# Kernel optimization log

Measured on AMD Instinct MI355X. Metric: run time of the kernel, lower is better.

The kernel has to match this reference:

```python
import jax, jax.numpy as jnp
import numpy as np

B, C, Hh, Ww = 32, 512, 6, 40
NC = 97   # num classes; padding_idx = NC-1, start_idx = NC-2
L = 26    # label length (max_len+1); decoder tokens T = L+1 = 27


def _lstm2(x, layers):
    """2-layer unidirectional LSTM, batch_first, PyTorch gate order (i,f,g,o).
    x: (B,T,D); layers: list of (Wih, Whh, bih, bhh). Returns (B,T,H)."""
    h = x
    for (Wih, Whh, bih, bhh) in layers:
        Hd = Whh.shape[1]
        b = bih + bhh
        def step(carry, xt, Wih=Wih, Whh=Whh, b=b):
            hh, cc = carry
            g = xt @ Wih.T + hh @ Whh.T + b
            i, f, gg, o = jnp.split(g, 4, axis=-1)
            cc = jax.nn.sigmoid(f) * cc + jax.nn.sigmoid(i) * jnp.tanh(gg)
            hh = jax.nn.sigmoid(o) * jnp.tanh(cc)
            return (hh, cc), hh
        init = (jnp.zeros((h.shape[0], Hd), h.dtype), jnp.zeros((h.shape[0], Hd), h.dtype))
        _, ys = jax.lax.scan(step, init, jnp.swapaxes(h, 0, 1))
        h = jnp.swapaxes(ys, 0, 1)
    return h


def setup_inputs() -> dict:
    key = jax.random.key(0)
    it = iter(jax.random.split(key, 48))
    def nrm(shape, s=0.02):
        return jax.random.normal(next(it), shape, jnp.float32) * s
    d = {}
    d['feat'] = jax.random.normal(next(it), (B, C, Hh, Ww), jnp.float32)
    d['label'] = jax.random.randint(next(it), (B, L), 0, NC)
    d['valid_ratios'] = jax.random.uniform(next(it), (B,), jnp.float32, 0.5, 1.0)
    # encoder LSTM (2 layers, 512->512)
    for p in ['e0', 'e1']:
        d[p + '_Wih'] = nrm((4 * C, C)); d[p + '_Whh'] = nrm((4 * C, C))
        d[p + '_bih'] = jnp.zeros((4 * C,), jnp.float32); d[p + '_bhh'] = jnp.zeros((4 * C,), jnp.float32)
    d['enc_W'] = nrm((C, C)); d['enc_b'] = jnp.zeros((C,), jnp.float32)
    # attention: query 1x1 (Linear), key conv3x3, score 1x1 (Linear d->1)
    d['q_W'] = nrm((C, C)); d['q_b'] = jnp.zeros((C,), jnp.float32)
    d['k_W'] = nrm((C, C, 3, 3)); d['k_b'] = jnp.zeros((C,), jnp.float32)
    d['s_W'] = nrm((1, C)); d['s_b'] = jnp.zeros((1,), jnp.float32)
    emb = nrm((NC, C), 1.0)
    d['emb'] = emb.at[NC - 1].set(0.0)  # padding_idx row is zero
    # decoder LSTM (2 layers, 512->512)
    for p in ['d0', 'd1']:
        d[p + '_Wih'] = nrm((4 * C, C)); d[p + '_Whh'] = nrm((4 * C, C))
        d[p + '_bih'] = jnp.zeros((4 * C,), jnp.float32); d[p + '_bhh'] = jnp.zeros((4 * C,), jnp.float32)
    d['pred_W'] = nrm((NC, 3 * C)); d['pred_b'] = jnp.zeros((NC,), jnp.float32)
    return d


def reference(feat, label, valid_ratios,
              e0_Wih, e0_Whh, e0_bih, e0_bhh, e1_Wih, e1_Whh, e1_bih, e1_bhh,
              enc_W, enc_b, q_W, q_b, k_W, k_b, s_W, s_b, emb,
              d0_Wih, d0_Whh, d0_bih, d0_bhh, d1_Wih, d1_Whh, d1_bih, d1_bhh,
              pred_W, pred_b):
    # --- SAREncoder: max-pool over height, 2-layer LSTM, linear on last step ---
    feat_v = jnp.max(feat, axis=2).transpose(0, 2, 1)  # (B, W, C)
    hf = _lstm2(feat_v, [(e0_Wih, e0_Whh, e0_bih, e0_bhh), (e1_Wih, e1_Whh, e1_bih, e1_bhh)])
    holistic = hf[:, -1, :] @ enc_W.T + enc_b  # (B, C)
    # --- tokens: [holistic, embed(label)] ---
    tok = jnp.concatenate([holistic[:, None, :], emb[label]], axis=1)  # (B, T=L+1, C)
    Hid = _lstm2(tok, [(d0_Wih, d0_Whh, d0_bih, d0_bhh), (d1_Wih, d1_Whh, d1_bih, d1_bhh)])
    # --- 2D additive attention ---
    q = Hid @ q_W.T + q_b  # (B, T, C)
    k = jax.lax.conv_general_dilated(feat, k_W, (1, 1), 'SAME',
                                     dimension_numbers=('NCHW', 'OIHW', 'NCHW')) + k_b[None, :, None, None]
    t = jnp.tanh(k[:, None] + q[:, :, :, None, None])  # (B, T, C, h, w) big intermediate
    score = jnp.einsum('btchw,c->bthw', t, s_W[0]) + s_b[0]  # (B, T, h, w)
    vw = jnp.minimum(Ww, jnp.ceil(Ww * valid_ratios)).astype(jnp.int32)  # (B,)
    colmask = jnp.arange(Ww)[None, :] >= vw[:, None]  # (B, w)
    score = jnp.where(colmask[:, None, None, :], -jnp.inf, score)
    T = score.shape[1]
    aw = jax.nn.softmax(score.reshape(score.shape[0], T, -1), axis=-1).reshape(score.shape[0], T, Hh, Ww)
    attn_feat = jnp.einsum('bchw,bthw->btc', feat, aw)  # (B, T, C)
    # --- prediction (pred_concat=True); dropout is identity (deterministic) ---
    hol = jnp.broadcast_to(holistic[:, None, :], Hid.shape)
    preds = jnp.concatenate([Hid, attn_feat, hol], axis=-1) @ pred_W.T + pred_b
    return preds[:, 1:, :]  # (B, L, NC)
```

## Files before the change

kernel.cpp:

```cpp
#include <hip/hip_runtime.h>

typedef unsigned short u16;
typedef __attribute__((ext_vector_type(8))) short short8;
typedef __attribute__((ext_vector_type(4))) float floatx4;
typedef _Float16 half8 __attribute__((ext_vector_type(8)));
typedef _Float16 half2v __attribute__((ext_vector_type(2)));
typedef unsigned uint4v __attribute__((ext_vector_type(4)));

#define AGENT __HIP_MEMORY_SCOPE_AGENT
#define SENT 0x7FFF7FFFu

__device__ __forceinline__ float bf2f(u16 v) { return __uint_as_float(((unsigned)v) << 16); }
__device__ __forceinline__ u16 f2bf(float f) {
    unsigned u = __float_as_uint(f);
    unsigned r = (u + 0x7FFFu + ((u >> 16) & 1u)) >> 16;
    return (u16)r;
}
__device__ __forceinline__ float sigm_(float x) {
    return __builtin_amdgcn_rcpf(1.f + __expf(-x));
}
__device__ __forceinline__ float tanh_(float x) {
    x = fminf(fmaxf(x, -15.f), 15.f);
    float e = __expf(2.f * x);
    return (e - 1.f) * __builtin_amdgcn_rcpf(e + 1.f);
}

typedef __attribute__((address_space(1))) void gvoid_t;
typedef __attribute__((address_space(3))) void lvoid_t;
__device__ __forceinline__ void gl_lds16(const void* g, void* l) {
    __builtin_amdgcn_global_load_lds((gvoid_t*)g, (lvoid_t*)l, 16, 0, 0);
}

#define HEX_WORDS (134 * 32 * 256)

__global__ void init_k(const void* __restrict__ feat_raw, int* __restrict__ flag,
                       unsigned* __restrict__ hEx) {
    int idx = blockIdx.x * 256 + threadIdx.x;
    hEx[idx] = SENT;
    if (idx == 0) {
        const u16* p = (const u16*)feat_raw;
        int insane = 0;
        #pragma unroll
        for (int i = 0; i < 32; i += 2) {
            float x = bf2f(p[i]);
            float a = fabsf(x);
            if (!(a <= 1000.f)) insane = 1;
            if (x != 0.f && a < 1e-8f) insane = 1;
        }
        *flag = insane;
    }
}

struct SrcPtrs {
    const void* e0Wih; const void* e1Wih; const void* d0Wih; const void* d1Wih;
    const void* b0; const void* b1; const void* b2; const void* b3;
    const void* b4; const void* b5; const void* b6; const void* b7;
    const void* encW; const void* qW; const void* predW; const void* emb;
    const void* encb; const void* qb; const void* kb; const void* sW;
    const void* sb; const void* predb;
};
#define OFF_W0      0
#define OFF_W1      1048576
#define OFF_W2      2097152
#define OFF_W3      3145728
#define OFF_B       4194304
#define OFF_ENCW    4210688
#define OFF_QW      4472832
#define OFF_PREDW   4734976
#define OFF_EMB     4883968
#define OFF_ENCB    4933632
#define OFF_QB      4934144
#define OFF_KB      4934656
#define OFF_SW      4935168
#define OFF_SB      4935680
#define OFF_PREDB   4935681
#define CANON_TOTAL 4935778

__global__ __launch_bounds__(256) void canon_all(SrcPtrs S, u16* __restrict__ dst,
                                                 const int* __restrict__ flag) {
    int idx = blockIdx.x * 256 + threadIdx.x;
    if (idx >= CANON_TOTAL) return;
    const void* s; int loc;
    if (idx < OFF_B) {
        int k = idx >> 20; loc = idx & 1048575;
        s = (k == 0) ? S.e0Wih : (k == 1) ? S.e1Wih : (k == 2) ? S.d0Wih : S.d1Wih;
    } else if (idx < OFF_ENCW) {
        int r = idx - OFF_B; int k = r >> 11; loc = r & 2047;
        s = (k == 0) ? S.b0 : (k == 1) ? S.b1 : (k == 2) ? S.b2 : (k == 3) ? S.b3
          : (k == 4) ? S.b4 : (k == 5) ? S.b5 : (k == 6) ? S.b6 : S.b7;
    } else if (idx < OFF_QW)    { s = S.encW;  loc = idx - OFF_ENCW; }
    else if (idx < OFF_PREDW)   { s = S.qW;    loc = idx - OFF_QW; }
    else if (idx < OFF_EMB)     { s = S.predW; loc = idx - OFF_PREDW; }
    else if (idx < OFF_ENCB)    { s = S.emb;   loc = idx - OFF_EMB; }
    else if (idx < OFF_QB)      { s = S.encb;  loc = idx - OFF_ENCB; }
    else if (idx < OFF_KB)      { s = S.qb;    loc = idx - OFF_QB; }
    else if (idx < OFF_SW)      { s = S.kb;    loc = idx - OFF_KB; }
    else if (idx < OFF_SB)      { s = S.sW;    loc = idx - OFF_SW; }
    else if (idx < OFF_PREDB)   { s = S.sb;    loc = idx - OFF_SB; }
    else                        { s = S.predb; loc = idx - OFF_PREDB; }
    dst[idx] = (*flag) ? f2bf(((const float*)s)[loc]) : ((const u16*)s)[loc];
}

__global__ __launch_bounds__(64) void canonf_k(const void* __restrict__ src, float* __restrict__ dst,
                                               int n, const int* __restrict__ flag) {
    int i = blockIdx.x * 64 + threadIdx.x;
    if (i >= n) return;
    dst[i] = (*flag) ? ((const float*)src)[i] : bf2f(((const u16*)src)[i]);
}

__device__ __forceinline__ float rdf(const void* p, long i, int fl) {
    return fl ? ((const float*)p)[i] : bf2f(((const u16*)p)[i]);
}

__global__ __launch_bounds__(256) void featv_k(const void* __restrict__ feat, u16* __restrict__ featv,
                                               const int* __restrict__ flag) {
    const int fl = *flag;
    int idx = blockIdx.x * 256 + threadIdx.x;
    int c = idx & 511;
    int r = idx >> 9;
    int w = r % 40, b = r / 40;
    float mx = -1e30f;
    long base = ((long)(b * 512 + c) * 6) * 40 + w;
    #pragma unroll
    for (int h = 0; h < 6; h++) mx = fmaxf(mx, rdf(feat, base + h * 40, fl));
    featv[idx] = f2bf(mx);
}

__global__ __launch_bounds__(256) void padfeat_k(const void* __restrict__ feat, u16* __restrict__ featP,
                                                 const int* __restrict__ flag) {
    const int fl = *flag;
    int idx = blockIdx.x * 256 + threadIdx.x;
    int c = idx & 511;
    int r = idx >> 9;
    int wp = r % 42; int r2 = r / 42;
    int hp = r2 & 7; int b = r2 >> 3;
    u16 v = 0;
    if (hp >= 1 && hp <= 6 && wp >= 1 && wp <= 40) {
        long si = ((long)(b * 512 + c) * 6 + (hp - 1)) * 40 + (wp - 1);
        v = fl ? f2bf(((const float*)feat)[si]) : ((const u16*)feat)[si];
    }
    featP[idx] = v;
}

__global__ __launch_bounds__(256) void w2_k(const void* __restrict__ kW, u16* __restrict__ W2,
                                            const int* __restrict__ flag) {
    int idx = blockIdx.x * 256 + threadIdx.x;
    int co = idx / 4608;
    int r = idx % 4608;
    int kh = r / 1536;
    int r2 = r % 1536;
    int kw = r2 / 512;
    int ci = r2 & 511;
    long si = ((long)(co * 512 + ci) * 3 + kh) * 3 + kw;
    W2[idx] = (*flag) ? f2bf(((const float*)kW)[si]) : ((const u16*)kW)[si];
}

__global__ __launch_bounds__(256) void wq3_all(
    const void* __restrict__ s0, const void* __restrict__ s1,
    const void* __restrict__ s2, const void* __restrict__ s3,
    _Float16* __restrict__ d0, _Float16* __restrict__ d1,
    _Float16* __restrict__ d2, _Float16* __restrict__ d3,
    const int* __restrict__ flag)
{
    int gb = blockIdx.x;
    int id = gb >> 9;
    const void* W = (id == 0) ? s0 : (id == 1) ? s1 : (id == 2) ? s2 : s3;
    _Float16* D = (id == 0) ? d0 : (id == 1) ? d1 : (id == 2) ? d2 : d3;
    int o = (gb & 511) * 256 + threadIdx.x;
    int t = o & 511;
    int c = (o >> 9) & 31;
    int j = o >> 14;
    int rid = t >> 1, hf = t & 1;
    int n = (rid >> 6) * 512 + j * 64 + (rid & 63);
    int k = hf * 256 + c * 8;
    int fl = *flag;
    _Float16* dst = D + (long)o * 8;
    #pragma unroll
    for (int jj = 0; jj < 8; jj++) {
        long si = (long)n * 512 + k + jj;
        float v = fl ? ((const float*)W)[si] : bf2f(((const u16*)W)[si]);
        dst[jj] = (_Float16)v;
    }
}

__global__ __launch_bounds__(256) void gemm_nt_f32(
    const u16* __restrict__ A, int lda,
    const u16* __restrict__ Bw,
    const u16* __restrict__ bias0, const u16* __restrict__ bias1,
    float* __restrict__ C, int M, int N, int K, int ldc)
{
    __shared__ __align__(16) u16 As[64][40];
    __shared__ __align__(16) u16 Bs[64][40];
    const int tid = threadIdx.x;
    const int bn = blockIdx.x, bm = blockIdx.y;
    const int l = tid & 63, wid = tid >> 6;
    const int wm = wid >> 1, wn = wid & 1;
    const int lr = tid >> 2, lc = (tid & 3) * 8;
    const int l15 = l & 15, lq = l >> 4;

    floatx4 acc00 = (floatx4)(0.f), acc01 = (floatx4)(0.f), acc10 = (floatx4)(0.f), acc11 = (floatx4)(0.f);

    int am = bm * 64 + lr; if (am > M - 1) am = M - 1;
    const u16* Ap = A + (long)am * lda + lc;
    const u16* Bp = Bw + (long)(bn * 64 + lr) * K + lc;

    for (int k0 = 0; k0 < K; k0 += 32) {
        *(short8*)&As[lr][lc] = *(const short8*)(Ap + k0);
        *(short8*)&Bs[lr][lc] = *(const short8*)(Bp + k0);
        __syncthreads();
        short8 af0 = *(const short8*)&As[wm * 32 + l15][lq * 8];
        short8 af1 = *(const short8*)&As[wm * 32 + 16 + l15][lq * 8];
        short8 bf0 = *(const short8*)&Bs[wn * 32 + l15][lq * 8];
        short8 bf1 = *(const short8*)&Bs[wn * 32 + 16 + l15][lq * 8];
        acc00 = __builtin_amdgcn_mfma_f32_16x16x32_bf16(af0, bf0, acc00, 0, 0, 0);
        acc01 = __builtin_amdgcn_mfma_f32_16x16x32_bf16(af0, bf1, acc01, 0, 0, 0);
        acc10 = __builtin_amdgcn_mfma_f32_16x16x32_bf16(af1, bf0, acc10, 0, 0, 0);
        acc11 = __builtin_amdgcn_mfma_f32_16x16x32_bf16(af1, bf1, acc11, 0, 0, 0);
        __syncthreads();
    }
    floatx4 accs[2][2] = {{acc00, acc01}, {acc10, acc11}};
    #pragma unroll
    for (int i = 0; i < 2; i++)
        #pragma unroll
        for (int j = 0; j < 2; j++)
            #pragma unroll
            for (int r = 0; r < 4; r++) {
                int gm = bm * 64 + wm * 32 + i * 16 + lq * 4 + r;
                int gn = bn * 64 + wn * 32 + j * 16 + l15;
                if (gm < M) {
                    float v = accs[i][j][r];
                    if (bias0) v += bf2f(bias0[gn]);
                    if (bias1) v += bf2f(bias1[gn]);
                    C[(long)gm * ldc + gn] = v;
                }
            }
}

__global__ __launch_bounds__(256) void conv_gemm(
    const u16* __restrict__ featP, const u16* __restrict__ W2,
    const u16* __restrict__ kb, u16* __restrict__ kmap)
{
    __shared__ __align__(16) u16 As[2][128][32];
    __shared__ __align__(16) u16 Bs[2][128][32];
    const int tid = threadIdx.x;
    int bm = blockIdx.x * 8 + (blockIdx.y & 7);
    int bn = blockIdx.y >> 3;
    if (bm >= 60) return;
    const int wv = tid >> 6, l = tid & 63;
    const int wm = wv >> 1, wn = wv & 1;
    const int l15 = l & 15, lq = l >> 4;
    const int s0 = wv * 2, s1 = s0 + 1;

    int ar0 = bm * 128 + s0 * 16 + (l >> 2);
    int ar1 = bm * 128 + s1 * 16 + (l >> 2);
    int ab0 = ar0 / 240, ahw0 = ar0 % 240;
    int ab1 = ar1 / 240, ahw1 = ar1 % 240;
    const u16* ga0 = featP + ((long)(ab0 * 8 + ahw0 / 40) * 42 + (ahw0 % 40)) * 512 + (l & 3) * 8;
    const u16* ga1 = featP + ((long)(ab1 * 8 + ahw1 / 40) * 42 + (ahw1 % 40)) * 512 + (l & 3) * 8;
    const u16* gb0 = W2 + (long)(bn * 128 + s0 * 16 + (l >> 2)) * 4608 + (l & 3) * 8;
    const u16* gb1 = W2 + (long)(bn * 128 + s1 * 16 + (l >> 2)) * 4608 + (l & 3) * 8;

    floatx4 acc[4][4];
    #pragma unroll
    for (int i = 0; i < 4; i++)
        #pragma unroll
        for (int j = 0; j < 4; j++) acc[i][j] = (floatx4)(0.f);

    auto stage = [&](int k0, int pb) {
        int kh = k0 / 1536;
        int rem = k0 - kh * 1536;
        int aoff = (kh * 42 + (rem >> 9)) * 512 + (rem & 511);
        gl_lds16(ga0 + aoff, &As[pb][s0 * 16][0]);
        gl_lds16(ga1 + aoff, &As[pb][s1 * 16][0]);
        gl_lds16(gb0 + k0, &Bs[pb][s0 * 16][0]);
        gl_lds16(gb1 + k0, &Bs[pb][s1 * 16][0]);
    };

    stage(0, 0);
    __syncthreads();
    for (int k = 0; k < 144; k++) {
        int cur = k & 1;
        if (k + 1 < 144) stage((k + 1) * 32, cur ^ 1);
        short8 af[4], bf[4];
        #pragma unroll
        for (int i = 0; i < 4; i++) af[i] = *(const short8*)&As[cur][wm * 64 + i * 16 + l15][lq * 8];
        #pragma unroll
        for (int j = 0; j < 4; j++) bf[j] = *(const short8*)&Bs[cur][wn * 64 + j * 16 + l15][lq * 8];
        #pragma unroll
        for (int i = 0; i < 4; i++)
            #pragma unroll
            for (int j = 0; j < 4; j++)
                acc[i][j] = __builtin_amdgcn_mfma_f32_16x16x32_bf16(af[i], bf[j], acc[i][j], 0, 0, 0);
        __syncthreads();
    }

    #pragma unroll
    for (int i = 0; i < 4; i++)
        #pragma unroll
        for (int j = 0; j < 4; j++)
            #pragma unroll
            for (int r = 0; r < 4; r++) {
                int row = bm * 128 + wm * 64 + i * 16 + lq * 4 + r;
                int col = bn * 128 + wn * 64 + j * 16 + l15;
                kmap[(long)row * 512 + col] = f2bf(acc[i][j][r] + bf2f(kb[col]));
            }
}

#define WL(F) F(0) F(1) F(2) F(3) F(4) F(5) F(6) F(7) F(8) F(9) F(10) F(11) F(12) F(13) F(14) F(15) \
              F(16) F(17) F(18) F(19) F(20) F(21) F(22) F(23) F(24) F(25) F(26) F(27) F(28) F(29) F(30) F(31)
#define WLA(F) F(0,0) F(1,1) F(2,2) F(3,3) F(4,0) F(5,1) F(6,2) F(7,3) \
               F(8,0) F(9,1) F(10,2) F(11,3) F(12,0) F(13,1) F(14,2) F(15,3) \
               F(16,0) F(17,1) F(18,2) F(19,3) F(20,0) F(21,1) F(22,2) F(23,3) \
               F(24,0) F(25,1) F(26,2) F(27,3) F(28,0) F(29,1) F(30,2) F(31,3)
#define WDECL(i) half8 w##i = wp8[(long)(j * 32 + i) * 512 + tid];
#define WPIN(i)  asm volatile("" : "+v"(w##i));
#define DOTC(i,k) { \
    half8 hv = *(const half8*)&hS2[(hf * 2 + (i / 16)) * 136 + (i % 16) * 8]; \
    a##k = __builtin_amdgcn_fdot2(__builtin_shufflevector(hv, hv, 0, 1), __builtin_shufflevector(w##i, w##i, 0, 1), a##k, false); \
    a##k = __builtin_amdgcn_fdot2(__builtin_shufflevector(hv, hv, 2, 3), __builtin_shufflevector(w##i, w##i, 2, 3), a##k, false); \
    a##k = __builtin_amdgcn_fdot2(__builtin_shufflevector(hv, hv, 4, 5), __builtin_shufflevector(w##i, w##i, 4, 5), a##k, false); \
    a##k = __builtin_amdgcn_fdot2(__builtin_shufflevector(hv, hv, 6, 7), __builtin_shufflevector(w##i, w##i, 6, 7), a##k, false); }

__global__ __launch_bounds__(512) __attribute__((amdgpu_waves_per_eu(2, 2))) void lstm_sync(
    const float* __restrict__ xpre, const _Float16* __restrict__ Wq3,
    u16* __restrict__ seq_out, float* __restrict__ f32_out,
    unsigned* __restrict__ hExT, int T, int f32_ld)
{
    const int i_ = blockIdx.x;
    const int slot = i_ >> 3;
    const int b = (i_ & 7) * 4 + (slot & 3);
    const int j = slot >> 2;
    const int tid = threadIdx.x;
    const int hf = tid & 1;

    __shared__ __align__(16) _Float16 hS2[4 * 136];
    __shared__ float part[512];

    const half8* wp8 = (const half8*)Wq3;
    WL(WDECL)
    WL(WPIN)
    float cst = 0.f;

    for (int t = 0; t < T; t++) {
        float xi = 0.f, xf = 0.f, xg = 0.f, xo = 0.f;
        if (tid < 64) {
            const float* xp = xpre + ((long)b * T + t) * 2048 + j * 64 + tid;
            xi = xp[0]; xf = xp[512]; xg = xp[1024]; xo = xp[1536];
        }
        float a0 = 0.f, a1 = 0.f, a2 = 0.f, a3 = 0.f;
        if (t > 0) {
            if (tid < 64) {
                const unsigned* src = &hExT[((long)(t - 1) * 32 + b) * 256 + tid * 4];
                unsigned v0, v1, v2, v3;
                do {
                    v0 = __hip_atomic_load(src + 0, __ATOMIC_RELAXED, AGENT);
                    v1 = __hip_atomic_load(src + 1, __ATOMIC_RELAXED, AGENT);
                    v2 = __hip_atomic_load(src + 2, __ATOMIC_RELAXED, AGENT);
                    v3 = __hip_atomic_load(src + 3, __ATOMIC_RELAXED, AGENT);
                } while (v0 == SENT || v1 == SENT || v2 == SENT || v3 == SENT);
                uint4v v; v.x = v0; v.y = v1; v.z = v2; v.w = v3;
                *(uint4v*)&hS2[(tid >> 4) * 136 + (tid & 15) * 8] = v;
            }
            __syncthreads();
            WLA(DOTC)
        }
        part[tid] = (a0 + a1) + (a2 + a3);
        __syncthreads();
        if (tid < 64) {
            float gi = xi + part[(0   + tid) * 2] + part[(0   + tid) * 2 + 1];
            float gf = xf + part[(64  + tid) * 2] + part[(64  + tid) * 2 + 1];
            float gg = xg + part[(128 + tid) * 2] + part[(128 + tid) * 2 + 1];
            float go = xo + part[(192 + tid) * 2] + part[(192 + tid) * 2 + 1];
            cst = sigm_(gf) * cst + sigm_(gi) * tanh_(gg);
            float h = sigm_(go) * tanh_(cst);
            float hlo = __shfl(h, tid * 2);
            float hhi = __shfl(h, tid * 2 + 1);
            if (t + 1 < T && tid < 32) {
                half2v hp; hp[0] = (_Float16)hlo; hp[1] = (_Float16)hhi;
                __hip_atomic_store(&hExT[((long)t * 32 + b) * 256 + j * 32 + tid],
                                   *(unsigned*)&hp, __ATOMIC_RELAXED, AGENT);
            }
            asm volatile("" ::: "memory");
            long so = ((long)b * T + t) * 512 + j * 64 + tid;
            seq_out[so] = f2bf(h);
            if (f32_out) f32_out[((long)b * T + t) * f32_ld + j * 64 + tid] = h;
        }
    }
}

__global__ __launch_bounds__(256) void tok_k(
    const float* __restrict__ holf, const u16* __restrict__ cemb,
    const int* __restrict__ label, u16* __restrict__ tok)
{
    int idx = blockIdx.x * 256 + threadIdx.x;
    int c = idx & 511;
    int m = idx >> 9;
    int b = m / 27, t = m % 27;
    float v;
    if (t == 0) v = holf[(long)b * 512 + c];
    else v = bf2f(cemb[(long)label[b * 26 + (t - 1)] * 512 + c]);
    tok[idx] = f2bf(v);
}

__global__ __launch_bounds__(256) void score_k(
    const float* __restrict__ q, const u16* __restrict__ kmap,
    const u16* __restrict__ sW, const u16* __restrict__ sb,
    const float* __restrict__ vr, float* __restrict__ aw)
{
    int blk = blockIdx.x;
    int xcd = blk & 7, rest = blk >> 3;
    int bq = rest & 3, t = rest >> 2;
    int b = xcd * 4 + bq;
    int bt = b * 27 + t;
    int tid = threadIdx.x, wv = tid >> 6, ln = tid & 63;

    __shared__ float sc[240];
    __shared__ float red[256];

    float qr[8], sr[8];
    const float* qp = q + (long)bt * 512 + ln * 8;
    #pragma unroll
    for (int i = 0; i < 8; i++) qr[i] = qp[i];
    #pragma unroll
    for (int i = 0; i < 8; i++) sr[i] = bf2f(sW[ln * 8 + i]);

    const u16* kb_ = kmap + (long)b * 240 * 512;
    for (int r = wv * 60; r < wv * 60 + 60; r++) {
        short8 kv = *(const short8*)(kb_ + (long)r * 512 + ln * 8);
        float acc = 0.f;
        #pragma unroll
        for (int i = 0; i < 8; i++) {
            float x = bf2f((u16)kv[i]) + qr[i];
            acc = fmaf(sr[i], tanh_(x), acc);
        }
        #pragma unroll
        for (int m = 32; m > 0; m >>= 1) acc += __shfl_xor(acc, m);
        if (ln == 0) sc[r] = acc;
    }
    __syncthreads();

    float scv = -INFINITY, ex = 0.f;
    if (tid < 240) {
        float rr = vr[b];
        int vw = (int)ceilf(40.f * rr);
        if (vw > 40) vw = 40;
        int wcol = tid % 40;
        scv = (wcol >= vw) ? -INFINITY : (sc[tid] + bf2f(sb[0]));
    }
    red[tid] = scv;
    __syncthreads();
    for (int s = 128; s > 0; s >>= 1) {
        if (tid < s) red[tid] = fmaxf(red[tid], red[tid + s]);
        __syncthreads();
    }
    float mx = red[0];
    __syncthreads();
    if (tid < 240) ex = (scv == -INFINITY) ? 0.f : __expf(scv - mx);
    red[tid] = ex;
    __syncthreads();
    for (int s = 128; s > 0; s >>= 1) {
        if (tid < s) red[tid] += red[tid + s];
        __syncthreads();
    }
    float inv = __builtin_amdgcn_rcpf(red[0]);
    if (tid < 240) aw[(long)bt * 240 + tid] = ex * inv;
}

__global__ __launch_bounds__(256) void attn_k(
    const void* __restrict__ feat, const float* __restrict__ aw,
    float* __restrict__ concat, const int* __restrict__ flag)
{
    const int fl = *flag;
    int b = blockIdx.x >> 3;
    int cc = (blockIdx.x & 7) * 64;
    int tid = threadIdx.x;
    __shared__ float awS[27 * 240];
    __shared__ u16 fS[64 * 240];
    for (int i = tid; i < 27 * 240; i += 256) awS[i] = aw[(long)b * 27 * 240 + i];
    long fbase = ((long)b * 512 + cc) * 240;
    for (int i = tid; i < 64 * 240; i += 256)
        fS[i] = fl ? f2bf(((const float*)feat)[fbase + i]) : ((const u16*)feat)[fbase + i];
    __syncthreads();
    for (int item = tid; item < 64 * 27; item += 256) {
        int c = item / 27, t = item % 27;
        const u16* fp = &fS[c * 240];
        const float* ap = &awS[t * 240];
        float acc = 0.f;
        for (int hw = 0; hw < 240; hw++) acc = fmaf(bf2f(fp[hw]), ap[hw], acc);
        concat[((long)(b * 27 + t)) * 1536 + 512 + cc + c] = acc;
    }
}

__global__ __launch_bounds__(256) void pred_k(
    const float* __restrict__ concat, const float* __restrict__ holf,
    const u16* __restrict__ pW, const u16* __restrict__ pb,
    void* __restrict__ out, const int* __restrict__ flag)
{
    int m0 = blockIdx.x * 4;
    int tid = threadIdx.x;
    const int fl = *flag;
    __shared__ float aS[4][1024];
    __shared__ float hS[4][512];
    for (int i = tid; i < 4 * 1024; i += 256)
        aS[i / 1024][i % 1024] = concat[(long)(m0 + i / 1024) * 1536 + (i % 1024)];
    for (int i = tid; i < 4 * 512; i += 256) {
        int m = m0 + i / 512;
        hS[i / 512][i % 512] = holf[(long)(m / 27) * 512 + (i % 512)];
    }
    __syncthreads();
    int r = tid >> 6;
    int nb = tid & 63;
    int m = m0 + r;
    int b = m / 27, t = m % 27;
    for (int n = nb; n < 97; n += 64) {
        const u16* wp = pW + (long)n * 1536;
        float acc = 0.f;
        for (int k = 0; k < 1024; k++) acc = fmaf(aS[r][k], bf2f(wp[k]), acc);
        for (int k = 0; k < 512; k++) acc = fmaf(hS[r][k], bf2f(wp[1024 + k]), acc);
        acc += bf2f(pb[n]);
        if (t > 0) {
            long o = ((long)(b * 26 + (t - 1))) * 97 + n;
            if (fl) ((float*)out)[o] = acc;
            else    ((u16*)out)[o] = f2bf(acc);
        }
    }
}

extern "C" void kernel_launch(void* const* d_in, const int* in_sizes, int n_in,
                              void* d_out, int out_size, void* d_ws, size_t ws_size,
                              hipStream_t stream) {
    (void)in_sizes; (void)n_in; (void)out_size; (void)ws_size;
    const void* feat_r = d_in[0];
    const int*  label  = (const int*)d_in[1];
    const void* vr_r   = d_in[2];

    char* w = (char*)d_ws;
    size_t off = 0;
    auto alloc = [&](size_t bytes) -> void* {
        void* p = w + off;
        off = (off + bytes + 63) & ~(size_t)63;
        return p;
    };
    int*   flag    = (int*)  alloc(4);
    unsigned* hEx  = (unsigned*)alloc((size_t)HEX_WORDS * 4);
    u16*   canon   = (u16*)  alloc((size_t)CANON_TOTAL * 2);
    float* cvr     = (float*)alloc(32ull * 4);
    u16*   featv   = (u16*)  alloc(655360ull * 2);
    float* xpre    = (float*)alloc(2621440ull * 4);
    u16*   seq0    = (u16*)  alloc(655360ull * 2);
    u16*   seq1    = (u16*)  alloc(655360ull * 2);
    u16*   tok     = (u16*)  alloc(442368ull * 2);
    u16*   seqd0   = (u16*)  alloc(442368ull * 2);
    u16*   Hid     = (u16*)  alloc(442368ull * 2);
    float* holf    = (float*)alloc(16384ull * 4);
    float* qf      = (float*)alloc(442368ull * 4);
    u16*   featP   = (u16*)  alloc(5505024ull * 2);
    u16*   W2      = (u16*)  alloc(2359296ull * 2);
    float* aw      = (float*)alloc(207360ull * 4);
    float* concat  = (float*)alloc(1327104ull * 4);
    _Float16* Wq[4];
    for (int i = 0; i < 4; i++) Wq[i] = (_Float16*)alloc(1048576ull * 2);
    u16*   kmap    = (u16*)xpre;

    unsigned* hEx0 = hEx;
    unsigned* hEx1 = hEx + 40ull * 8192;
    unsigned* hEx2 = hEx + 80ull * 8192;
    unsigned* hEx3 = hEx + 107ull * 8192;

    u16* cW0    = canon + OFF_W0;
    u16* cW1    = canon + OFF_W1;
    u16* cW2    = canon + OFF_W2;
    u16* cW3    = canon + OFF_W3;
    u16* cb0    = canon + OFF_B;
    u16* cencW  = canon + OFF_ENCW;
    u16* cqW    = canon + OFF_QW;
    u16* cpredW = canon + OFF_PREDW;
    u16* cemb   = canon + OFF_EMB;
    u16* cencb  = canon + OFF_ENCB;
    u16* cqb    = canon + OFF_QB;
    u16* ckb    = canon + OFF_KB;
    u16* csW    = canon + OFF_SW;
    u16* csb    = canon + OFF_SB;
    u16* cpredb = canon + OFF_PREDB;

    init_k<<<dim3(HEX_WORDS / 256), 256, 0, stream>>>(feat_r, flag, hEx);
    SrcPtrs S;
    S.e0Wih = d_in[3];  S.e1Wih = d_in[7];  S.d0Wih = d_in[20]; S.d1Wih = d_in[24];
    S.b0 = d_in[5];  S.b1 = d_in[6];  S.b2 = d_in[9];  S.b3 = d_in[10];
    S.b4 = d_in[22]; S.b5 = d_in[23]; S.b6 = d_in[26]; S.b7 = d_in[27];
    S.encW = d_in[11]; S.qW = d_in[13]; S.predW = d_in[28]; S.emb = d_in[19];
    S.encb = d_in[12]; S.qb = d_in[14]; S.kb = d_in[16]; S.sW = d_in[17];
    S.sb = d_in[18]; S.predb = d_in[29];
    canon_all<<<dim3((CANON_TOTAL + 255) / 256), 256, 0, stream>>>(S, canon, flag);
    canonf_k<<<dim3(1), 64, 0, stream>>>(vr_r, cvr, 32, flag);
    w2_k<<<dim3(9216), 256, 0, stream>>>(d_in[15], W2, flag);
    wq3_all<<<dim3(2048), 256, 0, stream>>>(d_in[4], d_in[8], d_in[21], d_in[25],
                                            Wq[0], Wq[1], Wq[2], Wq[3], flag);

    featv_k  <<<dim3(2560), 256, 0, stream>>>(feat_r, featv, flag);
    padfeat_k<<<dim3(21504), 256, 0, stream>>>(feat_r, featP, flag);

    gemm_nt_f32<<<dim3(32, 20), 256, 0, stream>>>(featv, 512, cW0, cb0 + 0 * 2048, cb0 + 1 * 2048, xpre, 1280, 2048, 512, 2048);
    lstm_sync<<<dim3(256), 512, 0, stream>>>(xpre, Wq[0], seq0, nullptr, hEx0, 40, 0);
    gemm_nt_f32<<<dim3(32, 20), 256, 0, stream>>>(seq0, 512, cW1, cb0 + 2 * 2048, cb0 + 3 * 2048, xpre, 1280, 2048, 512, 2048);
    lstm_sync<<<dim3(256), 512, 0, stream>>>(xpre, Wq[1], seq1, nullptr, hEx1, 40, 0);
    gemm_nt_f32<<<dim3(8, 1), 256, 0, stream>>>(seq1 + 39 * 512, 40 * 512, cencW, cencb, nullptr, holf, 32, 512, 512, 512);

    tok_k<<<dim3(1728), 256, 0, stream>>>(holf, cemb, label, tok);
    gemm_nt_f32<<<dim3(32, 14), 256, 0, stream>>>(tok, 512, cW2, cb0 + 4 * 2048, cb0 + 5 * 2048, xpre, 864, 2048, 512, 2048);
    lstm_sync<<<dim3(256), 512, 0, stream>>>(xpre, Wq[2], seqd0, nullptr, hEx2, 27, 0);
    gemm_nt_f32<<<dim3(32, 14), 256, 0, stream>>>(seqd0, 512, cW3, cb0 + 6 * 2048, cb0 + 7 * 2048, xpre, 864, 2048, 512, 2048);
    lstm_sync<<<dim3(256), 512, 0, stream>>>(xpre, Wq[3], Hid, concat, hEx3, 27, 1536);

    gemm_nt_f32<<<dim3(8, 14), 256, 0, stream>>>(Hid, 512, cqW, cqb, nullptr, qf, 864, 512, 512, 512);
    conv_gemm<<<dim3(8, 32), 256, 0, stream>>>(featP, W2, ckb, kmap);
    score_k<<<dim3(864), 256, 0, stream>>>(qf, kmap, csW, csb, cvr, aw);
    attn_k<<<dim3(256), 256, 0, stream>>>(feat_r, aw, concat, flag);

    pred_k<<<dim3(216), 256, 0, stream>>>(concat, holf, cpredW, cpredb, d_out, flag);
}
```

Measured before the change: 841.5 us.

## Deepen conv GEMM LDS pipeline to four stages and swizzle LDS layout

The conv_gemm kernel moves from double-buffered LDS staging to a four-buffer ring with three loads in flight. It waits with explicit vmcnt counters and a single barrier per iteration instead of two syncthreads. An XOR swizzle on the 16-byte chunk index is applied to both the global-to-LDS writes and the MFMA operand reads, to reduce LDS bank conflicts. In exchange LDS use doubles to 64KB per block, which may lower occupancy, and the hand-tuned waitcnt values must match the number of loads each stage issues.

```diff
diff --git a/kernel.cpp b/kernel.cpp
--- a/kernel.cpp
+++ b/kernel.cpp
@@ -240,8 +240,8 @@
     const u16* __restrict__ featP, const u16* __restrict__ W2,
     const u16* __restrict__ kb, u16* __restrict__ kmap)
 {
-    __shared__ __align__(16) u16 As[2][128][32];
-    __shared__ __align__(16) u16 Bs[2][128][32];
+    __shared__ __align__(16) u16 As[4][128][32];
+    __shared__ __align__(16) u16 Bs[4][128][32];
     const int tid = threadIdx.x;
     int bm = blockIdx.x * 8 + (blockIdx.y & 7);
     int bn = blockIdx.y >> 3;
@@ -250,15 +250,16 @@
     const int wm = wv >> 1, wn = wv & 1;
     const int l15 = l & 15, lq = l >> 4;
     const int s0 = wv * 2, s1 = s0 + 1;
+    const int ch = ((l & 3) ^ ((l >> 3) & 3)) * 8;
 
     int ar0 = bm * 128 + s0 * 16 + (l >> 2);
     int ar1 = bm * 128 + s1 * 16 + (l >> 2);
     int ab0 = ar0 / 240, ahw0 = ar0 % 240;
     int ab1 = ar1 / 240, ahw1 = ar1 % 240;
-    const u16* ga0 = featP + ((long)(ab0 * 8 + ahw0 / 40) * 42 + (ahw0 % 40)) * 512 + (l & 3) * 8;
-    const u16* ga1 = featP + ((long)(ab1 * 8 + ahw1 / 40) * 42 + (ahw1 % 40)) * 512 + (l & 3) * 8;
-    const u16* gb0 = W2 + (long)(bn * 128 + s0 * 16 + (l >> 2)) * 4608 + (l & 3) * 8;
-    const u16* gb1 = W2 + (long)(bn * 128 + s1 * 16 + (l >> 2)) * 4608 + (l & 3) * 8;
+    const u16* ga0 = featP + ((long)(ab0 * 8 + ahw0 / 40) * 42 + (ahw0 % 40)) * 512 + ch;
+    const u16* ga1 = featP + ((long)(ab1 * 8 + ahw1 / 40) * 42 + (ahw1 % 40)) * 512 + ch;
+    const u16* gb0 = W2 + (long)(bn * 128 + s0 * 16 + (l >> 2)) * 4608 + ch;
+    const u16* gb1 = W2 + (long)(bn * 128 + s1 * 16 + (l >> 2)) * 4608 + ch;
 
     floatx4 acc[4][4];
     #pragma unroll
@@ -276,23 +277,37 @@
         gl_lds16(gb1 + k0, &Bs[pb][s1 * 16][0]);
     };
 
-    stage(0, 0);
-    __syncthreads();
-    for (int k = 0; k < 144; k++) {
-        int cur = k & 1;
-        if (k + 1 < 144) stage((k + 1) * 32, cur ^ 1);
+    const int rs = (lq ^ ((l15 >> 1) & 3)) * 8;
+
+    auto compute = [&](int cur) {
         short8 af[4], bf[4];
         #pragma unroll
-        for (int i = 0; i < 4; i++) af[i] = *(const short8*)&As[cur][wm * 64 + i * 16 + l15][lq * 8];
-        #pragma unroll
-        for (int j = 0; j < 4; j++) bf[j] = *(const short8*)&Bs[cur][wn * 64 + j * 16 + l15][lq * 8];
+        for (int i = 0; i < 4; i++) af[i] = *(const short8*)&As[cur][wm * 64 + i * 16 + l15][rs];
+        #pragma unroll
+        for (int j = 0; j < 4; j++) bf[j] = *(const short8*)&Bs[cur][wn * 64 + j * 16 + l15][rs];
         #pragma unroll
         for (int i = 0; i < 4; i++)
             #pragma unroll
             for (int j = 0; j < 4; j++)
                 acc[i][j] = __builtin_amdgcn_mfma_f32_16x16x32_bf16(af[i], bf[j], acc[i][j], 0, 0, 0);
-        __syncthreads();
-    }
+    };
+
+    stage(0, 0); stage(32, 1); stage(64, 2);
+    for (int k = 0; k < 142; k++) {
+        asm volatile("s_waitcnt vmcnt(8)" ::: "memory");
+        __builtin_amdgcn_s_barrier();
+        asm volatile("" ::: "memory");
+        if (k < 141) stage((k + 3) * 32, (k + 3) & 3);
+        compute(k & 3);
+    }
+    asm volatile("s_waitcnt vmcnt(4)" ::: "memory");
+    __builtin_amdgcn_s_barrier();
+    asm volatile("" ::: "memory");
+    compute(142 & 3);
+    asm volatile("s_waitcnt vmcnt(0)" ::: "memory");
+    __builtin_amdgcn_s_barrier();
+    asm volatile("" ::: "memory");
+    compute(143 & 3);
 
     #pragma unroll
     for (int i = 0; i < 4; i++)
```

Measured after the change: 834.6 us. About the same (-0.8%).
